# Performance work log

Hardware: AMD Instinct MI355X
Metric: run time of the kernel (lower is better)

The kernel has to match this reference:

```python
import jax, jax.numpy as jnp
import numpy as np

N_ITER = 4
D = 768  # word_emb_dim == sent_dim of both CrossAttentionBlocks


def setup_inputs() -> dict:
    key = jax.random.key(0)
    ks = jax.random.split(key, 6)
    N_S, N_F = 16384, 4096
    return {
        "sents_emb": jax.random.normal(ks[0], (N_S, D), jnp.float32),
        "func_embed": jax.random.normal(ks[1], (N_F, D), jnp.float32),
        "Wv_f2s": jax.random.normal(ks[2], (D, D), jnp.float32) * 0.02,
        "bv_f2s": jax.random.normal(ks[3], (D,), jnp.float32) * 0.02,
        "Wv_s2f": jax.random.normal(ks[4], (D, D), jnp.float32) * 0.02,
        "bv_s2f": jax.random.normal(ks[5], (D,), jnp.float32) * 0.02,
    }


def reference(sents_emb, func_embed, Wv_f2s, bv_f2s, Wv_s2f, bv_s2f):
    scale = 1.0 / jnp.sqrt(jnp.asarray(D, sents_emb.dtype))
    sents_hid, func_hid = sents_emb, func_embed
    z = None
    for _ in range(N_ITER):  # small fixed iteration count, sequential dependency
        # func2sent: query=sents_hid, key=func_hid, value=W_v(func_hid)
        func_val = func_hid @ Wv_f2s.T + bv_f2s              # [N_f, D]
        z = scale * (sents_hid @ func_hid.T)                  # [N_s, N_f] logits (returned)
        att = jax.nn.softmax(z, axis=1)
        sents_hid = sents_hid + att @ func_val                # [N_s, D]
        # sent2func: query=func_hid, key=sents_hid, value=W_v(sents_hid)
        sent_val = sents_hid @ Wv_s2f.T + bv_s2f              # [N_s, D]
        z2 = scale * (func_hid @ sents_hid.T)                 # [N_f, N_s]
        func_hid = func_hid + jax.nn.softmax(z2, axis=1) @ sent_val
    return (sents_hid, func_hid, z)
```

## Files before the change

### kernel.cpp

```cpp
#include <hip/hip_runtime.h>
#include <stdint.h>

typedef __attribute__((ext_vector_type(8))) short s16x8;
typedef __attribute__((ext_vector_type(8))) unsigned short u16x8;
typedef __attribute__((ext_vector_type(4))) unsigned short u16x4;
typedef __attribute__((ext_vector_type(4))) float f32x4;

__device__ inline unsigned short f2b(float f){
  unsigned u = __builtin_bit_cast(unsigned, f);
  u = u + 0x7fffu + ((u >> 16) & 1u);
  return (unsigned short)(u >> 16);
}
__device__ inline float b2f(unsigned short h){
  unsigned u = ((unsigned)h) << 16;
  return __builtin_bit_cast(float, u);
}

typedef __attribute__((address_space(1))) const unsigned g_uint;
typedef __attribute__((address_space(3))) unsigned l_uint;

__device__ inline void gload_lds16(const void* g, void* l){
  __builtin_amdgcn_global_load_lds((g_uint*)reinterpret_cast<uintptr_t>(g),
                                   (l_uint*)reinterpret_cast<uintptr_t>(l), 16, 0, 0);
}

#define BARF() { __builtin_amdgcn_s_barrier(); asm volatile("" ::: "memory"); }

__device__ inline unsigned xcd_swizzle(unsigned lin, unsigned tot){
  const unsigned q = tot >> 3;
  return (lin & 7) * q + (lin >> 3);
}

template<int EPI>
__global__ __launch_bounds__(512, 2) void gemm256(
    const unsigned short* __restrict__ A, const unsigned short* __restrict__ B,
    int M, int N, int K, float scale,
    float* __restrict__ Cf, unsigned short* __restrict__ Cb,
    float* __restrict__ lsum)
{
  __shared__ __align__(16) char ldsraw[131072];
  const int tid  = threadIdx.x;
  const int wid  = tid >> 6, lane = tid & 63;
  const int wm   = wid >> 2, wn = wid & 3;

  const unsigned gx = gridDim.x, gy = gridDim.y;
  const unsigned lin = blockIdx.x + gx*blockIdx.y;
  const unsigned w   = xcd_swizzle(lin, gx*gy);
  const int bm = (w / gx) * 256, bn = (w % gx) * 256;

  const int NT = K >> 6;

  f32x4 acc[8][4] = {};

  auto stageA = [&](int T, int halfm){
    const int kb = T << 6;
    char* ldsb = ldsraw + ((T & 1) << 16) + halfm*16384;
    #pragma unroll
    for (int i = 0; i < 2; ++i){
      const int lr  = i*64 + (tid >> 3);
      const int gtr = halfm*64 + ((lr < 64) ? lr : lr + 64);
      const int sc  = ((tid & 7)*8) ^ ((lr & 7)*8);
      gload_lds16(A + (size_t)(bm + gtr)*K + kb + sc, ldsb + i*8192 + tid*16);
    }
  };
  auto stageB = [&](int T, int halfk){
    const int kb = (T << 6) + halfk*32;
    char* ldsb = ldsraw + ((T & 1) << 16) + 32768 + halfk*16384;
    #pragma unroll
    for (int i = 0; i < 2; ++i){
      const int lr = i*128 + (tid >> 2);
      const int sc = ((tid & 3)*8) ^ ((lr & 3)*8);
      gload_lds16(B + (size_t)(bn + lr)*K + kb + sc, ldsb + i*8192 + tid*16);
    }
  };

  const int fr = lane & 15;
  const int fo = (lane >> 4) << 4;
  const int amask = (fr & 7) << 4;
  const int bmask = (fr & 3) << 4;

  auto rdA = [&](const char* ldsS, int mh, int kk, s16x8* af){
    const char* ab = ldsS + mh*16384;
    #pragma unroll
    for (int mf = 0; mf < 4; ++mf){
      const int r = wm*64 + mf*16 + fr;
      af[mf] = *(const s16x8*)(ab + r*128 + ((kk*64 + fo) ^ amask));
    }
  };
  auto rdB = [&](const char* ldsS, int kk, s16x8* bf){
    const char* bb = ldsS + 32768 + kk*16384;
    #pragma unroll
    for (int nf = 0; nf < 4; ++nf){
      const int r = wn*64 + nf*16 + fr;
      bf[nf] = *(const s16x8*)(bb + r*64 + (fo ^ bmask));
    }
  };

  stageB(0, 0); stageA(0, 0); stageA(0, 1); stageB(0, 1);
  stageB(1, 0); stageA(1, 0);
  asm volatile("s_waitcnt vmcnt(4)" ::: "memory");
  BARF();

  for (int T = 0; T < NT; ++T){
    const char* ldsS = ldsraw + ((T & 1) << 16);
    s16x8 af[4], bf[4];
    rdA(ldsS, 0, 0, af); rdB(ldsS, 0, bf);
    if (T + 1 < NT) stageA(T + 1, 1);
    BARF();
    __builtin_amdgcn_s_setprio(1);
    #pragma unroll
    for (int mf = 0; mf < 4; ++mf)
      #pragma unroll
      for (int nf = 0; nf < 4; ++nf)
        acc[mf][nf] = __builtin_amdgcn_mfma_f32_16x16x32_bf16(af[mf], bf[nf], acc[mf][nf], 0, 0, 0);
    __builtin_amdgcn_s_setprio(0);
    BARF();
    rdA(ldsS, 1, 0, af);
    if (T + 1 < NT) stageB(T + 1, 1);
    BARF();
    __builtin_amdgcn_s_setprio(1);
    #pragma unroll
    for (int mf = 0; mf < 4; ++mf)
      #pragma unroll
      for (int nf = 0; nf < 4; ++nf)
        acc[4 + mf][nf] = __builtin_amdgcn_mfma_f32_16x16x32_bf16(af[mf], bf[nf], acc[4 + mf][nf], 0, 0, 0);
    __builtin_amdgcn_s_setprio(0);
    BARF();
    rdA(ldsS, 0, 1, af); rdB(ldsS, 1, bf);
    if (T + 2 < NT) stageB(T + 2, 0);
    BARF();
    __builtin_amdgcn_s_setprio(1);
    #pragma unroll
    for (int mf = 0; mf < 4; ++mf)
      #pragma unroll
      for (int nf = 0; nf < 4; ++nf)
        acc[mf][nf] = __builtin_amdgcn_mfma_f32_16x16x32_bf16(af[mf], bf[nf], acc[mf][nf], 0, 0, 0);
    __builtin_amdgcn_s_setprio(0);
    BARF();
    rdA(ldsS, 1, 1, af);
    if (T + 2 < NT) stageA(T + 2, 0);
    BARF();
    __builtin_amdgcn_s_setprio(1);
    #pragma unroll
    for (int mf = 0; mf < 4; ++mf)
      #pragma unroll
      for (int nf = 0; nf < 4; ++nf)
        acc[4 + mf][nf] = __builtin_amdgcn_mfma_f32_16x16x32_bf16(af[mf], bf[nf], acc[4 + mf][nf], 0, 0, 0);
    __builtin_amdgcn_s_setprio(0);
    if (T < NT - 2) { asm volatile("s_waitcnt vmcnt(4)" ::: "memory"); }
    else           { asm volatile("s_waitcnt vmcnt(0)" ::: "memory"); }
    BARF();
  }

  float* lds_rs = (float*)ldsraw;
  if (tid < 256) lds_rs[tid] = 0.f;
  __syncthreads();

  const int er0 = bm + wm*128 + ((lane >> 4) << 2);
  const int ec0 = bn + wn*64  + (lane & 15);
  #pragma unroll
  for (int mf = 0; mf < 8; ++mf){
    float rs[4] = {0.f, 0.f, 0.f, 0.f};
    #pragma unroll
    for (int nf = 0; nf < 4; ++nf){
      #pragma unroll
      for (int j = 0; j < 4; ++j){
        const int row = er0 + mf*16 + j;
        const int col = ec0 + nf*16;
        const size_t idx = (size_t)row * N + col;
        const float v = acc[mf][nf][j];
        unsigned short eb;
        if (EPI == 5){ eb = f2b(__expf(v * scale)); }
        else { const float zz = v * scale; Cf[idx] = zz; eb = f2b(__expf(zz)); }
        Cb[idx] = eb;
        rs[j] += b2f(eb);
      }
    }
    #pragma unroll
    for (int o = 8; o; o >>= 1){
      #pragma unroll
      for (int j = 0; j < 4; ++j) rs[j] += __shfl_xor(rs[j], o, 64);
    }
    if ((lane & 15) == 0){
      const int rbase = wm*128 + mf*16 + ((lane >> 4) << 2);
      #pragma unroll
      for (int j = 0; j < 4; ++j) atomicAdd(&lds_rs[rbase + j], rs[j]);
    }
  }
  __syncthreads();
  if (tid < 256) atomicAdd(&lsum[bm + tid], lds_rs[tid]);
}

template<int EPI>
__global__ __launch_bounds__(256, 4) void gemm_bt(
    const unsigned short* __restrict__ A, const unsigned short* __restrict__ B,
    int M, int N, int KS, float scale, const float* __restrict__ bias,
    const float* __restrict__ linv,
    float* __restrict__ Cf, unsigned short* __restrict__ Cb)
{
  __shared__ unsigned short As[128*64];
  __shared__ unsigned short Bs[128*64];
  const int tid  = threadIdx.x;
  const int wid  = tid >> 6, lane = tid & 63;
  const int wr   = wid >> 1, wc = wid & 1;

  const unsigned gx = gridDim.x, gy = gridDim.y;
  const unsigned lin = blockIdx.x + gx*(blockIdx.y + gy*blockIdx.z);
  const unsigned w   = xcd_swizzle(lin, gx*gy*gridDim.z);
  const unsigned bxs = w % gx;
  const unsigned rest = w / gx;
  const unsigned bys = rest % gy;
  const unsigned bzs = rest / gy;

  const int bm   = bys * 128, bn = bxs * 128;
  const int kb   = bzs * KS, ke = kb + KS;

  f32x4 acc[4][4] = {};

  const int l8   = lane >> 3;
  const int scol = ((((lane & 7) << 4) ^ (l8 << 4)) >> 1);
  const int Klead = gridDim.z * KS;

  const unsigned short* Ag[4]; const unsigned short* Bg[4];
  unsigned short* Al[4]; unsigned short* Bl[4];
  #pragma unroll
  for (int i = 0; i < 4; ++i){
    const int row = wid*32 + i*8 + l8;
    Ag[i] = A + (size_t)(bm + row) * Klead + scol;
    Bg[i] = B + (size_t)(bn + row) * Klead + scol;
    Al[i] = As + (wid*4 + i) * 512;
    Bl[i] = Bs + (wid*4 + i) * 512;
  }

  const int fr    = lane & 15;
  const int fk    = (lane >> 4) << 4;
  const int amask = (fr & 7) << 4;

  for (int k0 = kb; k0 < ke; k0 += 64){
    if (k0 != kb) __syncthreads();
    #pragma unroll
    for (int i = 0; i < 4; ++i){
      gload_lds16(Ag[i] + k0, Al[i]);
      gload_lds16(Bg[i] + k0, Bl[i]);
    }
    __syncthreads();
    #pragma unroll
    for (int kk = 0; kk < 2; ++kk){
      s16x8 af[4], bf[4];
      #pragma unroll
      for (int m = 0; m < 4; ++m){
        const int row = (wr << 6) + m*16 + fr;
        const int off = row*128 + (((kk << 6) + fk) ^ amask);
        af[m] = *(const s16x8*)((const char*)As + off);
      }
      #pragma unroll
      for (int n = 0; n < 4; ++n){
        const int row = (wc << 6) + n*16 + fr;
        const int off = row*128 + (((kk << 6) + fk) ^ amask);
        bf[n] = *(const s16x8*)((const char*)Bs + off);
      }
      #pragma unroll
      for (int m = 0; m < 4; ++m)
        #pragma unroll
        for (int n = 0; n < 4; ++n)
          acc[m][n] = __builtin_amdgcn_mfma_f32_16x16x32_bf16(af[m], bf[n], acc[m][n], 0, 0, 0);
    }
  }

  const int gr0 = bm + (wr << 6) + ((lane >> 4) << 2);
  const int gc0 = bn + (wc << 6) + (lane & 15);
  const size_t pbase = (size_t)bzs * M * N;
  #pragma unroll
  for (int m = 0; m < 4; ++m){
    #pragma unroll
    for (int j = 0; j < 4; ++j){
      const int row = gr0 + m*16 + j;
      const float li = (EPI == 7) ? linv[row] : 0.f;
      #pragma unroll
      for (int n = 0; n < 4; ++n){
        const int col = gc0 + n*16;
        const size_t idx = (size_t)row * N + col;
        const float v = acc[m][n][j];
        if      (EPI == 2) Cb[idx] = f2b(v + bias[row]);
        else if (EPI == 4) Cf[pbase + idx] = v;
        else if (EPI == 7){ const float o = Cf[idx] + li * v; Cf[idx] = o; Cb[idx] = f2b(o); }
      }
    }
  }
}

__global__ __launch_bounds__(256) void inv_k(const float* __restrict__ lsum,
                                             float* __restrict__ linv, int n)
{
  const int i = blockIdx.x * 256 + threadIdx.x;
  if (i < n) linv[i] = 1.0f / lsum[i];
}

__global__ __launch_bounds__(256) void reduce_splitk(
    const float* __restrict__ P, int S, size_t stride4,
    const float* __restrict__ linv, int d4,
    float* __restrict__ Cf, unsigned short* __restrict__ Cb, int n4)
{
  const int i = blockIdx.x * 256 + threadIdx.x;
  if (i >= n4) return;
  f32x4 s = {0.f, 0.f, 0.f, 0.f};
  for (int k = 0; k < S; ++k) s += ((const f32x4*)P)[(size_t)k * stride4 + i];
  const float li = linv[i / d4];
  f32x4 r = ((const f32x4*)Cf)[i];
  r += s * li;
  ((f32x4*)Cf)[i] = r;
  u16x4 o;
  o[0] = f2b(r[0]); o[1] = f2b(r[1]); o[2] = f2b(r[2]); o[3] = f2b(r[3]);
  ((u16x4*)Cb)[i] = o;
}

__global__ void cvt8(const float* __restrict__ src, float* __restrict__ dstf,
                     unsigned short* __restrict__ dstb, int n8)
{
  const int i = blockIdx.x * 256 + threadIdx.x;
  if (i >= n8) return;
  const f32x4 a = ((const f32x4*)src)[2*i];
  const f32x4 b = ((const f32x4*)src)[2*i + 1];
  if (dstf){ ((f32x4*)dstf)[2*i] = a; ((f32x4*)dstf)[2*i + 1] = b; }
  u16x8 o;
  o[0]=f2b(a[0]); o[1]=f2b(a[1]); o[2]=f2b(a[2]); o[3]=f2b(a[3]);
  o[4]=f2b(b[0]); o[5]=f2b(b[1]); o[6]=f2b(b[2]); o[7]=f2b(b[3]);
  ((u16x8*)dstb)[i] = o;
}

extern "C" void kernel_launch(void* const* d_in, const int* in_sizes, int n_in,
                              void* d_out, int out_size, void* d_ws, size_t ws_size,
                              hipStream_t stream)
{
  (void)in_sizes; (void)n_in; (void)out_size; (void)ws_size;
  const float* sents = (const float*)d_in[0];
  const float* funcs = (const float*)d_in[1];
  const float* WvA   = (const float*)d_in[2];
  const float* bvA   = (const float*)d_in[3];
  const float* WvB   = (const float*)d_in[4];
  const float* bvB   = (const float*)d_in[5];

  const int NS = 16384, NF = 4096, D = 768;

  float* outS = (float*)d_out;
  float* outF = outS + (size_t)NS * D;
  float* outZ = outF + (size_t)NF * D;

  char* ws = (char*)d_ws;
  unsigned short* att = (unsigned short*)ws;  ws += (size_t)NS * NF * 2;
  unsigned short* z2  = att;
  unsigned short* sb  = (unsigned short*)ws;  ws += (size_t)NS * D * 2;
  unsigned short* fb  = (unsigned short*)ws;  ws += (size_t)NF * D * 2;
  unsigned short* fvT = (unsigned short*)ws;  ws += (size_t)D * NF * 2;
  unsigned short* svT = (unsigned short*)ws;  ws += (size_t)D * NS * 2;
  unsigned short* wA  = (unsigned short*)ws;  ws += (size_t)D * D * 2;
  unsigned short* wB  = (unsigned short*)ws;  ws += (size_t)D * D * 2;
  float* lsum = (float*)ws;  ws += (size_t)NS * 4;
  float* linv = (float*)ws;  ws += (size_t)NS * 4;
  float* Pbuf = (float*)ws;  ws += (size_t)NF * D * 4 * 4;

  const float scale = 0.036084391824351615f;

  cvt8<<<dim3((NS*D/8 + 255)/256), 256, 0, stream>>>(sents, outS, sb, NS*D/8);
  cvt8<<<dim3((NF*D/8 + 255)/256), 256, 0, stream>>>(funcs, outF, fb, NF*D/8);
  cvt8<<<dim3((D*D/8 + 255)/256),  256, 0, stream>>>(WvA, nullptr, wA, D*D/8);
  cvt8<<<dim3((D*D/8 + 255)/256),  256, 0, stream>>>(WvB, nullptr, wB, D*D/8);

  for (int it = 0; it < 4; ++it){
    gemm_bt<2><<<dim3(NF/128, D/128, 1), dim3(256), 0, stream>>>(wA, fb, D, NF, D, 0.f, bvA, nullptr, nullptr, fvT);
    hipMemsetAsync(lsum, 0, NS*4, stream);
    if (it < 3){
      gemm256<5><<<dim3(NF/256, NS/256), dim3(512), 0, stream>>>(sb, fb, NS, NF, D, scale, nullptr, att, lsum);
    } else {
      gemm256<6><<<dim3(NF/256, NS/256), dim3(512), 0, stream>>>(sb, fb, NS, NF, D, scale, outZ, att, lsum);
    }
    inv_k<<<dim3(NS/256), 256, 0, stream>>>(lsum, linv, NS);
    gemm_bt<7><<<dim3(D/128, NS/128, 1), dim3(256), 0, stream>>>(att, fvT, NS, D, NF, 0.f, nullptr, linv, outS, sb);
    gemm_bt<2><<<dim3(NS/128, D/128, 1), dim3(256), 0, stream>>>(wB, sb, D, NS, D, 0.f, bvB, nullptr, nullptr, svT);
    hipMemsetAsync(lsum, 0, NF*4, stream);
    gemm256<5><<<dim3(NS/256, NF/256), dim3(512), 0, stream>>>(fb, sb, NF, NS, D, scale, nullptr, z2, lsum);
    inv_k<<<dim3(NF/256), 256, 0, stream>>>(lsum, linv, NF);
    gemm_bt<4><<<dim3(D/128, NF/128, 4), dim3(256), 0, stream>>>(z2, svT, NF, D, 4096, 0.f, nullptr, nullptr, Pbuf, nullptr);
    reduce_splitk<<<dim3(NF*D/4/256), 256, 0, stream>>>(Pbuf, 4, (size_t)NF*D/4, linv, D/4, outF, fb, NF*D/4);
  }
}
```

Baseline: 2.205 ms.

## Run att@V GEMM with 256-tile pipelined kernel and drop inv_k launches

```diff
diff --git a/kernel.cpp b/kernel.cpp
--- a/kernel.cpp
+++ b/kernel.cpp
@@ -152,50 +152,69 @@
     BARF();
   }
 
-  float* lds_rs = (float*)ldsraw;
-  if (tid < 256) lds_rs[tid] = 0.f;
-  __syncthreads();
-
   const int er0 = bm + wm*128 + ((lane >> 4) << 2);
   const int ec0 = bn + wn*64  + (lane & 15);
-  #pragma unroll
-  for (int mf = 0; mf < 8; ++mf){
-    float rs[4] = {0.f, 0.f, 0.f, 0.f};
-    #pragma unroll
-    for (int nf = 0; nf < 4; ++nf){
+
+  if (EPI == 7){
+    #pragma unroll
+    for (int mf = 0; mf < 8; ++mf){
       #pragma unroll
       for (int j = 0; j < 4; ++j){
         const int row = er0 + mf*16 + j;
-        const int col = ec0 + nf*16;
-        const size_t idx = (size_t)row * N + col;
-        const float v = acc[mf][nf][j];
-        unsigned short eb;
-        if (EPI == 5){ eb = f2b(__expf(v * scale)); }
-        else { const float zz = v * scale; Cf[idx] = zz; eb = f2b(__expf(zz)); }
-        Cb[idx] = eb;
-        rs[j] += b2f(eb);
-      }
-    }
-    #pragma unroll
-    for (int o = 8; o; o >>= 1){
-      #pragma unroll
-      for (int j = 0; j < 4; ++j) rs[j] += __shfl_xor(rs[j], o, 64);
-    }
-    if ((lane & 15) == 0){
-      const int rbase = wm*128 + mf*16 + ((lane >> 4) << 2);
-      #pragma unroll
-      for (int j = 0; j < 4; ++j) atomicAdd(&lds_rs[rbase + j], rs[j]);
-    }
-  }
-  __syncthreads();
-  if (tid < 256) atomicAdd(&lsum[bm + tid], lds_rs[tid]);
+        const float li = 1.0f / lsum[row];
+        #pragma unroll
+        for (int nf = 0; nf < 4; ++nf){
+          const int col = ec0 + nf*16;
+          const size_t idx = (size_t)row * N + col;
+          const float o = Cf[idx] + li * acc[mf][nf][j];
+          Cf[idx] = o;
+          Cb[idx] = f2b(o);
+        }
+      }
+    }
+  } else {
+    float* lds_rs = (float*)ldsraw;
+    if (tid < 256) lds_rs[tid] = 0.f;
+    __syncthreads();
+
+    #pragma unroll
+    for (int mf = 0; mf < 8; ++mf){
+      float rs[4] = {0.f, 0.f, 0.f, 0.f};
+      #pragma unroll
+      for (int nf = 0; nf < 4; ++nf){
+        #pragma unroll
+        for (int j = 0; j < 4; ++j){
+          const int row = er0 + mf*16 + j;
+          const int col = ec0 + nf*16;
+          const size_t idx = (size_t)row * N + col;
+          const float v = acc[mf][nf][j];
+          unsigned short eb;
+          if (EPI == 5){ eb = f2b(__expf(v * scale)); }
+          else { const float zz = v * scale; Cf[idx] = zz; eb = f2b(__expf(zz)); }
+          Cb[idx] = eb;
+          rs[j] += b2f(eb);
+        }
+      }
+      #pragma unroll
+      for (int o = 8; o; o >>= 1){
+        #pragma unroll
+        for (int j = 0; j < 4; ++j) rs[j] += __shfl_xor(rs[j], o, 64);
+      }
+      if ((lane & 15) == 0){
+        const int rbase = wm*128 + mf*16 + ((lane >> 4) << 2);
+        #pragma unroll
+        for (int j = 0; j < 4; ++j) atomicAdd(&lds_rs[rbase + j], rs[j]);
+      }
+    }
+    __syncthreads();
+    if (tid < 256) atomicAdd(&lsum[bm + tid], lds_rs[tid]);
+  }
 }
 
 template<int EPI>
 __global__ __launch_bounds__(256, 4) void gemm_bt(
     const unsigned short* __restrict__ A, const unsigned short* __restrict__ B,
     int M, int N, int KS, float scale, const float* __restrict__ bias,
-    const float* __restrict__ linv,
     float* __restrict__ Cf, unsigned short* __restrict__ Cb)
 {
   __shared__ unsigned short As[128*64];
@@ -275,7 +294,6 @@
     #pragma unroll
     for (int j = 0; j < 4; ++j){
       const int row = gr0 + m*16 + j;
-      const float li = (EPI == 7) ? linv[row] : 0.f;
       #pragma unroll
       for (int n = 0; n < 4; ++n){
         const int col = gc0 + n*16;
@@ -283,29 +301,21 @@
         const float v = acc[m][n][j];
         if      (EPI == 2) Cb[idx] = f2b(v + bias[row]);
         else if (EPI == 4) Cf[pbase + idx] = v;
-        else if (EPI == 7){ const float o = Cf[idx] + li * v; Cf[idx] = o; Cb[idx] = f2b(o); }
-      }
-    }
-  }
-}
-
-__global__ __launch_bounds__(256) void inv_k(const float* __restrict__ lsum,
-                                             float* __restrict__ linv, int n)
-{
-  const int i = blockIdx.x * 256 + threadIdx.x;
-  if (i < n) linv[i] = 1.0f / lsum[i];
+      }
+    }
+  }
 }
 
 __global__ __launch_bounds__(256) void reduce_splitk(
     const float* __restrict__ P, int S, size_t stride4,
-    const float* __restrict__ linv, int d4,
+    const float* __restrict__ lsum, int d4,
     float* __restrict__ Cf, unsigned short* __restrict__ Cb, int n4)
 {
   const int i = blockIdx.x * 256 + threadIdx.x;
   if (i >= n4) return;
   f32x4 s = {0.f, 0.f, 0.f, 0.f};
   for (int k = 0; k < S; ++k) s += ((const f32x4*)P)[(size_t)k * stride4 + i];
-  const float li = linv[i / d4];
+  const float li = 1.0f / lsum[i / d4];
   f32x4 r = ((const f32x4*)Cf)[i];
   r += s * li;
   ((f32x4*)Cf)[i] = r;
@@ -356,7 +366,6 @@
   unsigned short* wA  = (unsigned short*)ws;  ws += (size_t)D * D * 2;
   unsigned short* wB  = (unsigned short*)ws;  ws += (size_t)D * D * 2;
   float* lsum = (float*)ws;  ws += (size_t)NS * 4;
-  float* linv = (float*)ws;  ws += (size_t)NS * 4;
   float* Pbuf = (float*)ws;  ws += (size_t)NF * D * 4 * 4;
 
   const float scale = 0.036084391824351615f;
@@ -367,20 +376,18 @@
   cvt8<<<dim3((D*D/8 + 255)/256),  256, 0, stream>>>(WvB, nullptr, wB, D*D/8);
 
   for (int it = 0; it < 4; ++it){
-    gemm_bt<2><<<dim3(NF/128, D/128, 1), dim3(256), 0, stream>>>(wA, fb, D, NF, D, 0.f, bvA, nullptr, nullptr, fvT);
+    gemm_bt<2><<<dim3(NF/128, D/128, 1), dim3(256), 0, stream>>>(wA, fb, D, NF, D, 0.f, bvA, nullptr, fvT);
     hipMemsetAsync(lsum, 0, NS*4, stream);
     if (it < 3){
       gemm256<5><<<dim3(NF/256, NS/256), dim3(512), 0, stream>>>(sb, fb, NS, NF, D, scale, nullptr, att, lsum);
     } else {
       gemm256<6><<<dim3(NF/256, NS/256), dim3(512), 0, stream>>>(sb, fb, NS, NF, D, scale, outZ, att, lsum);
     }
-    inv_k<<<dim3(NS/256), 256, 0, stream>>>(lsum, linv, NS);
-    gemm_bt<7><<<dim3(D/128, NS/128, 1), dim3(256), 0, stream>>>(att, fvT, NS, D, NF, 0.f, nullptr, linv, outS, sb);
-    gemm_bt<2><<<dim3(NS/128, D/128, 1), dim3(256), 0, stream>>>(wB, sb, D, NS, D, 0.f, bvB, nullptr, nullptr, svT);
+    gemm256<7><<<dim3(D/256, NS/256), dim3(512), 0, stream>>>(att, fvT, NS, D, NF, 0.f, outS, sb, lsum);
+    gemm_bt<2><<<dim3(NS/128, D/128, 1), dim3(256), 0, stream>>>(wB, sb, D, NS, D, 0.f, bvB, nullptr, svT);
     hipMemsetAsync(lsum, 0, NF*4, stream);
     gemm256<5><<<dim3(NS/256, NF/256), dim3(512), 0, stream>>>(fb, sb, NF, NS, D, scale, nullptr, z2, lsum);
-    inv_k<<<dim3(NF/256), 256, 0, stream>>>(lsum, linv, NF);
-    gemm_bt<4><<<dim3(D/128, NF/128, 4), dim3(256), 0, stream>>>(z2, svT, NF, D, 4096, 0.f, nullptr, nullptr, Pbuf, nullptr);
-    reduce_splitk<<<dim3(NF*D/4/256), 256, 0, stream>>>(Pbuf, 4, (size_t)NF*D/4, linv, D/4, outF, fb, NF*D/4);
-  }
-}
+    gemm_bt<4><<<dim3(D/128, NF/128, 4), dim3(256), 0, stream>>>(z2, svT, NF, D, 4096, 0.f, nullptr, Pbuf, nullptr);
+    reduce_splitk<<<dim3(NF*D/4/256), 256, 0, stream>>>(Pbuf, 4, (size_t)NF*D/4, lsum, D/4, outF, fb, NF*D/4);
+  }
+}
```

Measured after the change: 2.248 ms. Within noise of the previous version (+1.9%).
